# Performance work log

Hardware: AMD Instinct MI355X
Metric: run time of the kernel (lower is better)

The kernel has to match this reference:

```python
import jax, jax.numpy as jnp
import numpy as np

N_NODES = 50000
N_EDGES = 800000
IN_DIM = 128
OUT_DIM = 128
NUM_RELS = 8


def setup_inputs() -> dict:
    key = jax.random.key(0)
    k_feat, k_rel, k_w, k_src, k_dst, k_rt = jax.random.split(key, 6)
    feat = jax.random.normal(k_feat, (N_NODES, IN_DIM), dtype=jnp.float32)
    # xavier_uniform over (in_dim, out_dim) fan
    limit = float(np.sqrt(6.0 / (IN_DIM + OUT_DIM)))
    rel_emb = jax.random.uniform(k_rel, (NUM_RELS, IN_DIM, OUT_DIM), dtype=jnp.float32,
                                 minval=-limit, maxval=limit)
    edge_weight = jax.random.uniform(k_w, (N_EDGES,), dtype=jnp.float32)
    src = jax.random.randint(k_src, (N_EDGES,), 0, N_NODES, dtype=jnp.int32)
    dst = jax.random.randint(k_dst, (N_EDGES,), 0, N_NODES, dtype=jnp.int32)
    rel_type = jax.random.randint(k_rt, (N_EDGES,), 0, NUM_RELS, dtype=jnp.int32)
    return {"feat": feat, "rel_emb": rel_emb, "edge_weight": edge_weight,
            "src": src, "dst": dst, "rel_type": rel_type}


def reference(feat, rel_emb, edge_weight, src, dst, rel_type):
    # src_feat: [E, in] gather of source-node features
    src_feat = feat[src]
    num_rels = rel_emb.shape[0]
    # Equivalent to bmm(src_feat[:,None,:], rel_emb[rel_type]).squeeze(1)
    # but avoids materializing the [E, in, out] per-edge weight tensor:
    # loop over the small fixed relation set with masked accumulation.
    msg = jnp.zeros((src_feat.shape[0], rel_emb.shape[2]), dtype=src_feat.dtype)
    for r in range(num_rels):
        mask = (rel_type == r)[:, None]
        msg = msg + jnp.where(mask, src_feat @ rel_emb[r], jnp.zeros((), dtype=src_feat.dtype))
    msg = msg * edge_weight[:, None]
    # copy_e + sum aggregation onto destination nodes: [N, out]
    return jax.ops.segment_sum(msg, dst, num_segments=feat.shape[0])
```

## Files before the change

### kernel.cpp

```cpp
#include <hip/hip_runtime.h>
#include <stdint.h>

#define N_NODES   50000
#define N_EDGES   800000
#define IN_DIM    128
#define OUT_DIM   128
#define NUM_RELS  8
#define THREADS   256

typedef _Float16 half_t;
typedef _Float16 half2v __attribute__((ext_vector_type(2)));
typedef _Float16 half4v __attribute__((ext_vector_type(4)));
typedef _Float16 half8 __attribute__((ext_vector_type(8)));
typedef float floatx4 __attribute__((ext_vector_type(4)));


#define NBINS3    N_NODES
#define NB3       ((NBINS3 + 1023) / 1024)

#define WS_Y2     0
#define WS_OFF    102400000
#define WS_WT     102600064
#define WS_REC    102862208
#define WS_HIST2  109262208
#define WS_BSUM2  109462208
#define WS_NEED2  (size_t)109462464

#define WS_BASE   102862208
#define WS_WGT    106062208
#define WS_HIST   107662208
#define WS_BSUM   107862208
#define WS_NEED   (size_t)107862464

#define HIST_BLOCKS ((N_EDGES + 1023) / 1024)
__global__ void prep_hist_kernel(const float* __restrict__ rel_emb, half_t* __restrict__ WT,
                                 const int* __restrict__ dst, int* __restrict__ hist) {
    int b = blockIdx.x;
    if (b < 512) {
        int t = b * 256 + threadIdx.x;
        int r = t >> 14, k = (t >> 7) & 127, n = t & 127;
        WT[(size_t)((r << 7) | n) * 128 + k] = (half_t)rel_emb[t];
    } else {
        int i0 = (b - 512) * 1024 + threadIdx.x;
        int d[4];
        #pragma unroll
        for (int j = 0; j < 4; j++) {
            int i = i0 + j * 256;
            d[j] = (i < N_EDGES) ? dst[i] : -1;
        }
        #pragma unroll
        for (int j = 0; j < 4; j++)
            if (d[j] >= 0) atomicAdd(&hist[d[j]], 1);
    }
}

__global__ void scan1_kernel(const int* __restrict__ hist, int* __restrict__ bsum) {
    __shared__ int sh[256];
    int b = blockIdx.x, t = threadIdx.x;
    int i0 = b * 1024 + t * 4;
    int s = 0;
    #pragma unroll
    for (int j = 0; j < 4; j++) { int idx = i0 + j; if (idx < NBINS3) s += hist[idx]; }
    sh[t] = s; __syncthreads();
    for (int o = 128; o > 0; o >>= 1) { if (t < o) sh[t] += sh[t + o]; __syncthreads(); }
    if (t == 0) bsum[b] = sh[0];
}

__global__ void scan2_kernel(int* __restrict__ bsum, int* __restrict__ off) {
    __shared__ int sh[64];
    int t = threadIdx.x;
    int v = (t < NB3) ? bsum[t] : 0;
    sh[t] = v; __syncthreads();
    for (int o = 1; o < 64; o <<= 1) {
        int x = (t >= o) ? sh[t - o] : 0;
        __syncthreads();
        sh[t] += x;
        __syncthreads();
    }
    if (t < NB3) bsum[t] = sh[t] - v;
    if (t == 0) off[NBINS3] = N_EDGES;
}

__global__ void scan3_kernel(const int* __restrict__ hist, const int* __restrict__ boff,
                             int* __restrict__ off, int* __restrict__ cursors) {
    __shared__ int sh[256];
    int b = blockIdx.x, t = threadIdx.x;
    int i0 = b * 1024 + t * 4;
    int v[4]; int s = 0;
    #pragma unroll
    for (int j = 0; j < 4; j++) { int idx = i0 + j; v[j] = (idx < NBINS3) ? hist[idx] : 0; s += v[j]; }
    sh[t] = s; __syncthreads();
    for (int o = 1; o < 256; o <<= 1) {
        int x = (t >= o) ? sh[t - o] : 0;
        __syncthreads();
        sh[t] += x;
        __syncthreads();
    }
    int run = sh[t] - s + boff[b];
    #pragma unroll
    for (int j = 0; j < 4; j++) {
        int idx = i0 + j;
        if (idx < NBINS3) { off[idx] = run; cursors[idx] = run; }
        run += v[j];
    }
}

template<bool GUARD>
__device__ __forceinline__ void gemm_body(const float* __restrict__ feat,
                                          half_t* __restrict__ Ws,
                                          half_t* __restrict__ y2,
                                          int m0, int n0, int wave, int lane) {
    const int q = lane >> 4, l16 = lane & 15;
    const int wm0 = m0 + wave * 32;

    float4 fr[2][4][2];
    #pragma unroll
    for (int ms = 0; ms < 2; ms++) {
        int node = wm0 + ms * 16 + l16;
        const float* fb = feat + (size_t)node * 128 + q * 8;
        bool ok = !GUARD || node < N_NODES;
        #pragma unroll
        for (int kk = 0; kk < 4; kk++)
            #pragma unroll
            for (int h = 0; h < 2; h++) {
                float4 v = {0.f, 0.f, 0.f, 0.f};
                if (ok) v = *(const float4*)(fb + kk * 32 + h * 4);
                fr[ms][kk][h] = v;
            }
    }
    __syncthreads();

    half8 bf[2][4];
    #pragma unroll
    for (int ms = 0; ms < 2; ms++)
        #pragma unroll
        for (int kk = 0; kk < 4; kk++) {
            half8 hb;
            hb[0] = (half_t)fr[ms][kk][0].x; hb[1] = (half_t)fr[ms][kk][0].y;
            hb[2] = (half_t)fr[ms][kk][0].z; hb[3] = (half_t)fr[ms][kk][0].w;
            hb[4] = (half_t)fr[ms][kk][1].x; hb[5] = (half_t)fr[ms][kk][1].y;
            hb[6] = (half_t)fr[ms][kk][1].z; hb[7] = (half_t)fr[ms][kk][1].w;
            bf[ms][kk] = hb;
        }

    floatx4 acc[8][2];
    #pragma unroll
    for (int nt = 0; nt < 8; nt++)
        #pragma unroll
        for (int ms = 0; ms < 2; ms++) acc[nt][ms] = (floatx4){0.f, 0.f, 0.f, 0.f};

    #pragma unroll
    for (int kk = 0; kk < 4; kk++) {
        #pragma unroll
        for (int nt = 0; nt < 8; nt++) {
            int row = nt * 16 + l16;
            int phys = (kk * 4 + q) ^ (l16 & 7);
            half8 a = *(const half8*)(Ws + row * 128 + phys * 8);
            acc[nt][0] = __builtin_amdgcn_mfma_f32_16x16x32_f16(a, bf[0][kk], acc[nt][0], 0, 0, 0);
            acc[nt][1] = __builtin_amdgcn_mfma_f32_16x16x32_f16(a, bf[1][kk], acc[nt][1], 0, 0, 0);
        }
    }

    __syncthreads();
    #pragma unroll
    for (int nt = 0; nt < 8; nt++)
        #pragma unroll
        for (int ms = 0; ms < 2; ms++) {
            int nl = wave * 32 + ms * 16 + l16;
            int c  = nt * 4 + q;
            int p  = (c + nl) & 31;
            half4v hv;
            hv[0] = (half_t)acc[nt][ms][0]; hv[1] = (half_t)acc[nt][ms][1];
            hv[2] = (half_t)acc[nt][ms][2]; hv[3] = (half_t)acc[nt][ms][3];
            *(half4v*)(Ws + nl * 128 + p * 4) = hv;
        }
    #pragma unroll
    for (int i = 0; i < 8; i++) {
        int nl  = wave * 32 + i * 4 + (lane >> 4);
        int c16 = lane & 15;
        int p0 = (2 * c16 + nl) & 31;
        int p1 = (2 * c16 + 1 + nl) & 31;
        uint2 lo = *(const uint2*)(Ws + nl * 128 + p0 * 4);
        uint2 hi = *(const uint2*)(Ws + nl * 128 + p1 * 4);
        int node = m0 + nl;
        if (!GUARD || node < N_NODES) {
            uint4 v; v.x = lo.x; v.y = lo.y; v.z = hi.x; v.w = hi.y;
            *(uint4*)(y2 + (size_t)node * 1024 + n0 + c16 * 8) = v;
        }
    }
}

#define GEMM_BLOCKS 3128
__global__ __launch_bounds__(THREADS) void gemm_kernel(
    const float* __restrict__ feat, const half_t* __restrict__ WT,
    half_t* __restrict__ y2) {
    __shared__ half_t Ws[128 * 128];
    const int bid = blockIdx.x;
    const int t = threadIdx.x;

    int work = (bid & 7) * 391 + (bid >> 3);
    int mt = work >> 3, nt8 = work & 7;
    const int m0 = mt * 128, n0 = nt8 * 128;
    const int wave = t >> 6, lane = t & 63;

    for (int i = t; i < 2048; i += THREADS) {
        int row = i >> 4, lc = i & 15;
        int phys = lc ^ (row & 7);
        *(uint4*)&Ws[row * 128 + phys * 8] =
            *(const uint4*)(WT + (size_t)(n0 + row) * 128 + lc * 8);
    }
    if (m0 + 128 <= N_NODES)
        gemm_body<false>(feat, Ws, y2, m0, n0, wave, lane);
    else
        gemm_body<true>(feat, Ws, y2, m0, n0, wave, lane);
}

__global__ __launch_bounds__(THREADS) void scatter_pack_kernel(
    const int* __restrict__ dst, const int* __restrict__ src,
    const int* __restrict__ rel, const float* __restrict__ ew,
    int* __restrict__ cursors, uint2* __restrict__ rec) {
    const int t = threadIdx.x;
    int i0 = blockIdx.x * 1024 + t;
    int d[4], s[4], r[4]; float w[4];
    #pragma unroll
    for (int j = 0; j < 4; j++) {
        int i = i0 + j * 256;
        d[j] = (i < N_EDGES) ? dst[i] : -1;
        s[j] = 0; r[j] = 0; w[j] = 0.f;
        if (d[j] >= 0) { s[j] = src[i]; r[j] = rel[i]; w[j] = ew[i]; }
    }
    #pragma unroll
    for (int j = 0; j < 4; j++) {
        if (d[j] >= 0) {
            int pos = atomicAdd(&cursors[d[j]], 1);
            uint2 v;
            v.x = (unsigned)(s[j] * 1024 + r[j] * 128);
            v.y = __float_as_uint(w[j]);
            rec[pos] = v;
        }
    }
}

__global__ __launch_bounds__(THREADS) void gather_pack_kernel(
    const half_t* __restrict__ y2, const uint2* __restrict__ rec,
    const int* __restrict__ off, float* __restrict__ out) {
    int g = blockIdx.x * 4 + (threadIdx.x >> 6);
    int lane = threadIdx.x & 63;
    int q = lane >> 4, l16 = lane & 15;
    int beg = off[g], end = off[g + 1];
    const half_t* yb = y2 + l16 * 8;
    float a0[8], a1[8];
    #pragma unroll
    for (int j = 0; j < 8; j++) { a0[j] = 0.f; a1[j] = 0.f; }
    int e = beg;
    for (; e + 8 <= end; e += 8) {
        uint2 r0 = rec[e + q], r1 = rec[e + 4 + q];
        float w0 = __uint_as_float(r0.y), w1 = __uint_as_float(r1.y);
        half8 v0 = *(const half8*)(yb + r0.x);
        half8 v1 = *(const half8*)(yb + r1.x);
        #pragma unroll
        for (int j = 0; j < 8; j++) a0[j] += w0 * (float)v0[j];
        #pragma unroll
        for (int j = 0; j < 8; j++) a1[j] += w1 * (float)v1[j];
    }
    for (; e < end; e += 4) {
        int ee = e + q;
        unsigned b0 = 0; float w0 = 0.f;
        if (ee < end) { uint2 r0 = rec[ee]; b0 = r0.x; w0 = __uint_as_float(r0.y); }
        half8 v0 = *(const half8*)(yb + b0);
        #pragma unroll
        for (int j = 0; j < 8; j++) a0[j] += w0 * (float)v0[j];
    }
    #pragma unroll
    for (int j = 0; j < 8; j++) {
        float s = a0[j] + a1[j];
        s += __shfl_xor(s, 16);
        s += __shfl_xor(s, 32);
        a0[j] = s;
    }
    if (q == 0) {
        float4 o0, o1;
        o0.x = a0[0]; o0.y = a0[1]; o0.z = a0[2]; o0.w = a0[3];
        o1.x = a0[4]; o1.y = a0[5]; o1.z = a0[6]; o1.w = a0[7];
        float* ob = out + (size_t)g * 128 + l16 * 8;
        *(float4*)ob = o0;
        *(float4*)(ob + 4) = o1;
    }
}

__global__ __launch_bounds__(THREADS) void scatter_kernel(
    const int* __restrict__ dst, const int* __restrict__ src,
    const int* __restrict__ rel, const float* __restrict__ ew,
    int* __restrict__ cursors, int* __restrict__ base, half_t* __restrict__ wgt) {
    const int t = threadIdx.x;
    int i0 = blockIdx.x * 1024 + t;
    int d[4], s[4], r[4]; float w[4];
    #pragma unroll
    for (int j = 0; j < 4; j++) {
        int i = i0 + j * 256;
        d[j] = (i < N_EDGES) ? dst[i] : -1;
        s[j] = 0; r[j] = 0; w[j] = 0.f;
        if (d[j] >= 0) { s[j] = src[i]; r[j] = rel[i]; w[j] = ew[i]; }
    }
    #pragma unroll
    for (int j = 0; j < 4; j++) {
        if (d[j] >= 0) {
            int pos = atomicAdd(&cursors[d[j]], 1);
            base[pos] = s[j] * 1024 + r[j] * 128;
            wgt[pos] = (half_t)w[j];
        }
    }
}

__global__ __launch_bounds__(THREADS) void gather_kernel(
    const half_t* __restrict__ y2, const int* __restrict__ base,
    const half_t* __restrict__ wgt, const int* __restrict__ off,
    float* __restrict__ out) {
    int g = blockIdx.x * 4 + (threadIdx.x >> 6);
    int lane = threadIdx.x & 63;
    int q = lane >> 4, l16 = lane & 15;
    int beg = off[g], end = off[g + 1];
    const half_t* yb = y2 + l16 * 8;
    float a0[8], a1[8];
    #pragma unroll
    for (int j = 0; j < 8; j++) { a0[j] = 0.f; a1[j] = 0.f; }
    int e = beg;
    for (; e + 8 <= end; e += 8) {
        int e0 = e + q, e1 = e + 4 + q;
        int b0 = base[e0], b1 = base[e1];
        float w0 = (float)wgt[e0], w1 = (float)wgt[e1];
        half8 v0 = *(const half8*)(yb + b0);
        half8 v1 = *(const half8*)(yb + b1);
        #pragma unroll
        for (int j = 0; j < 8; j++) a0[j] += w0 * (float)v0[j];
        #pragma unroll
        for (int j = 0; j < 8; j++) a1[j] += w1 * (float)v1[j];
    }
    for (; e < end; e += 4) {
        int ee = e + q;
        int b0 = 0; float w0 = 0.f;
        if (ee < end) { b0 = base[ee]; w0 = (float)wgt[ee]; }
        half8 v0 = *(const half8*)(yb + b0);
        #pragma unroll
        for (int j = 0; j < 8; j++) a0[j] += w0 * (float)v0[j];
    }
    #pragma unroll
    for (int j = 0; j < 8; j++) {
        float s = a0[j] + a1[j];
        s += __shfl_xor(s, 16);
        s += __shfl_xor(s, 32);
        a0[j] = s;
    }
    if (q == 0) {
        float4 o0, o1;
        o0.x = a0[0]; o0.y = a0[1]; o0.z = a0[2]; o0.w = a0[3];
        o1.x = a0[4]; o1.y = a0[5]; o1.z = a0[6]; o1.w = a0[7];
        float* ob = out + (size_t)g * 128 + l16 * 8;
        *(float4*)ob = o0;
        *(float4*)(ob + 4) = o1;
    }
}

__global__ void naive_kernel(const float* __restrict__ feat, const float* __restrict__ rel_emb,
                             const float* __restrict__ ew, const int* __restrict__ src,
                             const int* __restrict__ dst, const int* __restrict__ rel,
                             float* __restrict__ out) {
    int wave = (blockIdx.x * blockDim.x + threadIdx.x) >> 6;
    int lane = threadIdx.x & 63;
    if (wave >= N_EDGES) return;
    const float* f = feat + (size_t)src[wave] * IN_DIM;
    const float* W = rel_emb + (size_t)rel[wave] * IN_DIM * OUT_DIM;
    float w = ew[wave];
    float a0 = 0.f, a1 = 0.f;
    for (int k = 0; k < IN_DIM; k++) {
        float fv = f[k];
        a0 += fv * W[k * OUT_DIM + lane];
        a1 += fv * W[k * OUT_DIM + 64 + lane];
    }
    int d = dst[wave];
    atomicAdd(&out[(size_t)d * OUT_DIM + lane], a0 * w);
    atomicAdd(&out[(size_t)d * OUT_DIM + 64 + lane], a1 * w);
}

extern "C" void kernel_launch(void* const* d_in, const int* in_sizes, int n_in,
                              void* d_out, int out_size, void* d_ws, size_t ws_size,
                              hipStream_t stream) {
    const float* feat    = (const float*)d_in[0];
    const float* rel_emb = (const float*)d_in[1];
    const float* ew      = (const float*)d_in[2];
    const int*   src     = (const int*)d_in[3];
    const int*   dst     = (const int*)d_in[4];
    const int*   rel     = (const int*)d_in[5];
    float* out = (float*)d_out;

    if (ws_size >= WS_NEED2) {
        char* ws = (char*)d_ws;
        half_t* y2    = (half_t*)(ws + WS_Y2);
        int*    off   = (int*)(ws + WS_OFF);
        half_t* WT    = (half_t*)(ws + WS_WT);
        uint2*  rec   = (uint2*)(ws + WS_REC);
        int*    hist  = (int*)(ws + WS_HIST2);
        int*    bsum  = (int*)(ws + WS_BSUM2);

        hipMemsetAsync(hist, 0, (size_t)NBINS3 * 4, stream);
        prep_hist_kernel<<<512 + HIST_BLOCKS, THREADS, 0, stream>>>(rel_emb, WT, dst, hist);
        scan1_kernel<<<NB3, 256, 0, stream>>>(hist, bsum);
        scan2_kernel<<<1, 64, 0, stream>>>(bsum, off);
        scan3_kernel<<<NB3, 256, 0, stream>>>(hist, bsum, off, hist);
        scatter_pack_kernel<<<HIST_BLOCKS, THREADS, 0, stream>>>(dst, src, rel, ew, hist, rec);
        gemm_kernel<<<GEMM_BLOCKS, THREADS, 0, stream>>>(feat, WT, y2);
        gather_pack_kernel<<<N_NODES / 4, THREADS, 0, stream>>>(y2, rec, off, out);
    } else if (ws_size >= WS_NEED) {
        char* ws = (char*)d_ws;
        half_t* y2    = (half_t*)(ws + WS_Y2);
        int*    off   = (int*)(ws + WS_OFF);
        half_t* WT    = (half_t*)(ws + WS_WT);
        int*    basep = (int*)(ws + WS_BASE);
        half_t* wgt   = (half_t*)(ws + WS_WGT);
        int*    hist  = (int*)(ws + WS_HIST);
        int*    bsum  = (int*)(ws + WS_BSUM);

        hipMemsetAsync(hist, 0, (size_t)NBINS3 * 4, stream);
        prep_hist_kernel<<<512 + HIST_BLOCKS, THREADS, 0, stream>>>(rel_emb, WT, dst, hist);
        scan1_kernel<<<NB3, 256, 0, stream>>>(hist, bsum);
        scan2_kernel<<<1, 64, 0, stream>>>(bsum, off);
        scan3_kernel<<<NB3, 256, 0, stream>>>(hist, bsum, off, hist);
        scatter_kernel<<<HIST_BLOCKS, THREADS, 0, stream>>>(dst, src, rel, ew,
                                                            hist, basep, wgt);
        gemm_kernel<<<GEMM_BLOCKS, THREADS, 0, stream>>>(feat, WT, y2);
        gather_kernel<<<N_NODES / 4, THREADS, 0, stream>>>(y2, basep, wgt, off, out);
    } else {
        hipMemsetAsync(d_out, 0, (size_t)out_size * sizeof(float), stream);
        const long long total = (long long)N_EDGES * 64;
        const int blocks = (int)((total + THREADS - 1) / THREADS);
        naive_kernel<<<blocks, THREADS, 0, stream>>>(feat, rel_emb, ew, src, dst, rel, out);
    }
}
```

Before: 264.6 us.

## Record per-edge ranks in histogram pass and fuse scatter into GEMM kernel

The histogram pass now keeps the value returned by each atomicAdd as a per-edge rank. That rank is stored temporarily in the output buffer, which the final gather overwrites later. The separate scatter kernel, with its second round of atomics on the cursors, is removed. Each GEMM block now also handles 256 edges: it loads the edge fields before the GEMM and writes the packed record at off[dst]+rank afterwards, which saves a launch and a full atomic pass. In exchange, the GEMM kernel holds extra registers across its body, and the histogram kernel processes one edge per thread instead of four.

```diff
diff --git a/kernel.cpp b/kernel.cpp
--- a/kernel.cpp
+++ b/kernel.cpp
@@ -31,6 +31,23 @@
 #define WS_HIST   107662208
 #define WS_BSUM   107862208
 #define WS_NEED   (size_t)107862464
+
+#define EDGE_BLOCKS ((N_EDGES + 255) / 256)
+
+__global__ void prep_rank_kernel(const float* __restrict__ rel_emb, half_t* __restrict__ WT,
+                                 const int* __restrict__ dst, int* __restrict__ hist,
+                                 int* __restrict__ rank) {
+    int b = blockIdx.x;
+    if (b < 512) {
+        int t = b * 256 + threadIdx.x;
+        int r = t >> 14, k = (t >> 7) & 127, n = t & 127;
+        WT[(size_t)((r << 7) | n) * 128 + k] = (half_t)rel_emb[t];
+    } else {
+        int i = (b - 512) * 256 + threadIdx.x;
+        if (i < N_EDGES)
+            rank[i] = atomicAdd(&hist[dst[i]], 1);
+    }
+}
 
 #define HIST_BLOCKS ((N_EDGES + 1023) / 1024)
 __global__ void prep_hist_kernel(const float* __restrict__ rel_emb, half_t* __restrict__ WT,
@@ -191,12 +208,23 @@
 }
 
 #define GEMM_BLOCKS 3128
-__global__ __launch_bounds__(THREADS) void gemm_kernel(
+__global__ __launch_bounds__(THREADS) void gemm_scatter_kernel(
     const float* __restrict__ feat, const half_t* __restrict__ WT,
-    half_t* __restrict__ y2) {
+    half_t* __restrict__ y2,
+    const int* __restrict__ dst, const int* __restrict__ src,
+    const int* __restrict__ rel, const float* __restrict__ ew,
+    const int* __restrict__ rank, const int* __restrict__ off,
+    uint2* __restrict__ rec) {
     __shared__ half_t Ws[128 * 128];
     const int bid = blockIdx.x;
     const int t = threadIdx.x;
+
+    int ei = bid * 256 + t;
+    int ed = -1, es = 0, er = 0, rk = 0; float wv = 0.f;
+    if (ei < N_EDGES) {
+        ed = dst[ei]; es = src[ei]; er = rel[ei];
+        wv = ew[ei];  rk = rank[ei];
+    }
 
     int work = (bid & 7) * 391 + (bid >> 3);
     int mt = work >> 3, nt8 = work & 7;
@@ -213,31 +241,13 @@
         gemm_body<false>(feat, Ws, y2, m0, n0, wave, lane);
     else
         gemm_body<true>(feat, Ws, y2, m0, n0, wave, lane);
-}
-
-__global__ __launch_bounds__(THREADS) void scatter_pack_kernel(
-    const int* __restrict__ dst, const int* __restrict__ src,
-    const int* __restrict__ rel, const float* __restrict__ ew,
-    int* __restrict__ cursors, uint2* __restrict__ rec) {
-    const int t = threadIdx.x;
-    int i0 = blockIdx.x * 1024 + t;
-    int d[4], s[4], r[4]; float w[4];
-    #pragma unroll
-    for (int j = 0; j < 4; j++) {
-        int i = i0 + j * 256;
-        d[j] = (i < N_EDGES) ? dst[i] : -1;
-        s[j] = 0; r[j] = 0; w[j] = 0.f;
-        if (d[j] >= 0) { s[j] = src[i]; r[j] = rel[i]; w[j] = ew[i]; }
-    }
-    #pragma unroll
-    for (int j = 0; j < 4; j++) {
-        if (d[j] >= 0) {
-            int pos = atomicAdd(&cursors[d[j]], 1);
-            uint2 v;
-            v.x = (unsigned)(s[j] * 1024 + r[j] * 128);
-            v.y = __float_as_uint(w[j]);
-            rec[pos] = v;
-        }
+
+    if (ed >= 0) {
+        int pos = off[ed] + rk;
+        uint2 v;
+        v.x = (unsigned)(es * 1024 + er * 128);
+        v.y = __float_as_uint(wv);
+        rec[pos] = v;
     }
 }
 
@@ -286,6 +296,28 @@
         *(float4*)ob = o0;
         *(float4*)(ob + 4) = o1;
     }
+}
+
+__global__ __launch_bounds__(THREADS) void gemm_kernel(
+    const float* __restrict__ feat, const half_t* __restrict__ WT,
+    half_t* __restrict__ y2) {
+    __shared__ half_t Ws[128 * 128];
+    const int bid = blockIdx.x;
+    const int t = threadIdx.x;
+    int work = (bid & 7) * 391 + (bid >> 3);
+    int mt = work >> 3, nt8 = work & 7;
+    const int m0 = mt * 128, n0 = nt8 * 128;
+    const int wave = t >> 6, lane = t & 63;
+    for (int i = t; i < 2048; i += THREADS) {
+        int row = i >> 4, lc = i & 15;
+        int phys = lc ^ (row & 7);
+        *(uint4*)&Ws[row * 128 + phys * 8] =
+            *(const uint4*)(WT + (size_t)(n0 + row) * 128 + lc * 8);
+    }
+    if (m0 + 128 <= N_NODES)
+        gemm_body<false>(feat, Ws, y2, m0, n0, wave, lane);
+    else
+        gemm_body<true>(feat, Ws, y2, m0, n0, wave, lane);
 }
 
 __global__ __launch_bounds__(THREADS) void scatter_kernel(
@@ -401,14 +433,15 @@
         uint2*  rec   = (uint2*)(ws + WS_REC);
         int*    hist  = (int*)(ws + WS_HIST2);
         int*    bsum  = (int*)(ws + WS_BSUM2);
+        int*    rank  = (int*)d_out;
 
         hipMemsetAsync(hist, 0, (size_t)NBINS3 * 4, stream);
-        prep_hist_kernel<<<512 + HIST_BLOCKS, THREADS, 0, stream>>>(rel_emb, WT, dst, hist);
+        prep_rank_kernel<<<512 + EDGE_BLOCKS, THREADS, 0, stream>>>(rel_emb, WT, dst, hist, rank);
         scan1_kernel<<<NB3, 256, 0, stream>>>(hist, bsum);
         scan2_kernel<<<1, 64, 0, stream>>>(bsum, off);
         scan3_kernel<<<NB3, 256, 0, stream>>>(hist, bsum, off, hist);
-        scatter_pack_kernel<<<HIST_BLOCKS, THREADS, 0, stream>>>(dst, src, rel, ew, hist, rec);
-        gemm_kernel<<<GEMM_BLOCKS, THREADS, 0, stream>>>(feat, WT, y2);
+        gemm_scatter_kernel<<<GEMM_BLOCKS, THREADS, 0, stream>>>(feat, WT, y2, dst, src, rel,
+                                                                 ew, rank, off, rec);
         gather_pack_kernel<<<N_NODES / 4, THREADS, 0, stream>>>(y2, rec, off, out);
     } else if (ws_size >= WS_NEED) {
         char* ws = (char*)d_ws;
```

New measurement: 224.1 us. 15.3% less time.
